# Performance work log

Hardware: AMD Instinct MI355X
Metric: run time of the kernel (lower is better)

The kernel has to match this reference:

```python
import jax, jax.numpy as jnp
import numpy as np

B, D, U = 4096, 1024, 1024  # batch, complex input dim, units


def _bias(u):
    # unit_forget_bias: zeros with forget-gate slice (i,f,c,o ordering) set to 1
    return jnp.zeros((4 * u,), jnp.float32).at[u:2 * u].set(1.0)


def setup_inputs() -> dict:
    key = jax.random.key(0)
    ks = jax.random.split(key, 7)
    s = 0.02  # kernel init scale
    return {
        "inputs": jax.random.normal(ks[0], (B, 2 * D), jnp.float32),
        "h_tm1": jax.random.normal(ks[1], (B, 2 * U), jnp.float32),
        "c_tm1": jax.random.normal(ks[2], (B, 2 * U), jnp.float32),
        "real_kernel": s * jax.random.normal(ks[3], (D, 4 * U), jnp.float32),
        "imaginary_kernel": s * jax.random.normal(ks[4], (D, 4 * U), jnp.float32),
        "real_recurrent_kernel": s * jax.random.normal(ks[5], (U, 4 * U), jnp.float32),
        "imaginary_recurrent_kernel": s * jax.random.normal(ks[6], (U, 4 * U), jnp.float32),
        "real_bias": _bias(U),
        "imaginary_bias": _bias(U),
    }


def hard_sigmoid(x):
    # keras hard_sigmoid: clip(0.2*x + 0.5, 0, 1)
    return jnp.clip(0.2 * x + 0.5, 0.0, 1.0)


def reference(inputs, h_tm1, c_tm1, real_kernel, imaginary_kernel,
              real_recurrent_kernel, imaginary_recurrent_kernel,
              real_bias, imaginary_bias):
    d = real_kernel.shape[0]
    u = real_recurrent_kernel.shape[0]
    xr, xi = inputs[:, :d], inputs[:, d:]          # [B,D] real/imag
    hr, hi = h_tm1[:, :u], h_tm1[:, u:]            # [B,U]
    # x @ [[R,-I],[I,R]] == [xr@R + xi@I, xi@R - xr@I]; done once over all 4 gates
    zr = xr @ real_kernel + xi @ imaginary_kernel \
         + hr @ real_recurrent_kernel + hi @ imaginary_recurrent_kernel + real_bias      # [B,4U]
    zi = xi @ real_kernel - xr @ imaginary_kernel \
         + hi @ real_recurrent_kernel - hr @ imaginary_recurrent_kernel + imaginary_bias  # [B,4U]

    def gate(g):  # concatenated real|imag pre-activation for gate g (i,f,c,o)
        s = slice(g * u, (g + 1) * u)
        return jnp.concatenate([zr[:, s], zi[:, s]], axis=-1)  # [B,2U]

    i = hard_sigmoid(gate(0))
    f = hard_sigmoid(gate(1))
    c = f * c_tm1 + i * jnp.tanh(gate(2))
    o = hard_sigmoid(gate(3))
    h = o * jnp.tanh(c)
    return h, c
```

## Files before the change

kernel.cpp:

```cpp
#include <hip/hip_runtime.h>

typedef unsigned short u16;
typedef unsigned int   u32;

typedef __bf16 bf16x8 __attribute__((ext_vector_type(8)));
typedef float  f32x4  __attribute__((ext_vector_type(4)));

typedef const __attribute__((address_space(1))) u32 GAS;
typedef __attribute__((address_space(3))) u32 LAS;

__device__ __forceinline__ u16 f2bf(float f) {
  u32 u = __builtin_bit_cast(u32, f);
  return (u16)((u + 0x7FFFu + ((u >> 16) & 1u)) >> 16);
}

__global__ __launch_bounds__(256) void build_x_k(
    const float* __restrict__ inp, const float* __restrict__ h,
    u16* __restrict__ X4) {
  __shared__ float t[64 * 65];
  const int tid = threadIdx.x;
  const int tx = tid & 15, ty = tid >> 4;
  const int m0 = blockIdx.y * 64, k0 = blockIdx.x * 64;
  const int sel = k0 >> 10;
  const int kc = k0 & 1023;
  const float* s1 = (sel < 2) ? inp : h;
  const int c1 = (sel & 1) * 1024 + kc;
#pragma unroll
  for (int rr = 0; rr < 4; ++rr) {
    const int m = rr * 16 + ty;
    float4 v = *(const float4*)&s1[(size_t)(m0 + m) * 2048 + c1 + tx * 4];
    t[(tx * 4 + 0) * 65 + m] = v.x;
    t[(tx * 4 + 1) * 65 + m] = v.y;
    t[(tx * 4 + 2) * 65 + m] = v.z;
    t[(tx * 4 + 3) * 65 + m] = v.w;
  }
  __syncthreads();
#pragma unroll
  for (int rep = 0; rep < 2; ++rep) {
    const int cell = rep * 256 + tid;
    const int kblk = cell >> 6, m = cell & 63;
    union { u16 s[8]; uint4 v; } tmp;
#pragma unroll
    for (int i = 0; i < 8; ++i) tmp.s[i] = f2bf(t[(kblk * 8 + i) * 65 + m]);
    *(uint4*)&X4[((size_t)(k0 / 8 + kblk) * 4096 + m0 + m) * 8] = tmp.v;
  }
}

__global__ __launch_bounds__(256) void build_w_k(
    const float* __restrict__ Kr, const float* __restrict__ Ki,
    const float* __restrict__ Rr, const float* __restrict__ Ri,
    u16* __restrict__ W4) {
  __shared__ float t[4 * 1032];
  const int tid = threadIdx.x;
  const int tx = tid & 15, ty = tid >> 4;
  const int yb = blockIdx.y;
  const int hh = yb >> 6, jhi = yb & 63;
  const int k0 = blockIdx.x * 64;
  const int kq = k0 >> 10;
  const int krow = k0 & 1023;
  const int jbase = jhi * 16;
  const float* sA;
  float sg = 1.0f;
  if (hh == 0) {
    sA = (kq == 0) ? Kr : (kq == 1) ? Ki : (kq == 2) ? Rr : Ri;
  } else {
    sA = (kq == 0) ? Ki : (kq == 1) ? Kr : (kq == 2) ? Ri : Rr;
    if ((kq & 1) == 0) sg = -1.0f;
  }
#pragma unroll
  for (int g = 0; g < 4; ++g) {
    const int cs = g * 1024 + jbase + tx;
#pragma unroll
    for (int rr = 0; rr < 4; ++rr) {
      const int k = rr * 16 + ty;
      t[g * 1032 + k * 16 + tx] = sg * sA[(size_t)(krow + k) * 4096 + cs];
    }
  }
  __syncthreads();
#pragma unroll
  for (int rep = 0; rep < 2; ++rep) {
    const int cell = rep * 256 + tid;
    const int kblk = cell >> 6, n = cell & 63;
    const int g = n >> 4, jlo = n & 15;
    union { u16 s[8]; uint4 v; } tmp;
#pragma unroll
    for (int i = 0; i < 8; ++i)
      tmp.s[i] = f2bf(t[g * 1032 + (kblk * 8 + i) * 16 + jlo]);
    *(uint4*)&W4[((size_t)(k0 / 8 + kblk) * 8192 + (size_t)hh * 4096 +
                  (size_t)jhi * 64 + n) * 8] = tmp.v;
  }
}

#define NKT 64

__global__ __launch_bounds__(512, 2) void clstm_gemm_k(
    const u16* __restrict__ X4, const u16* __restrict__ W4,
    const float* __restrict__ cprev, const float* __restrict__ rb,
    const float* __restrict__ ib, float* __restrict__ out) {
  __shared__ __align__(16) u16 lds[10][8192];
  const int tid = threadIdx.x;
  const int lane = tid & 63, wave = tid >> 6;
  const int wr = wave >> 2, wc = wave & 3;
  const int orig = blockIdx.x;
  const int wg = (orig & 7) * 64 + (orig >> 3);
  const int mb = wg >> 5, nb = wg & 31;
  const int m0 = mb * 256, n0 = nb * 256;
  const u16* L = &lds[0][0];

  f32x4 acc[8][4] = {};

  auto stageA = [&](int ktile, int hf, int slot) {
    const u16* s = X4 + ((size_t)(ktile * 8 + wave) * 4096 + m0 + hf * 128 + lane) * 8;
    __builtin_amdgcn_global_load_lds((GAS*)s, (LAS*)&lds[slot][(wave * 128) * 8], 16, 0, 0);
    __builtin_amdgcn_global_load_lds((GAS*)(s + 512), (LAS*)&lds[slot][(wave * 128 + 64) * 8], 16, 0, 0);
  };
  auto stageB = [&](int ktile, int hf, int slot) {
    const u16* s = W4 + ((size_t)(ktile * 8 + wave) * 8192 + n0 + hf * 128 + lane) * 8;
    __builtin_amdgcn_global_load_lds((GAS*)s, (LAS*)&lds[slot][(wave * 128) * 8], 16, 0, 0);
    __builtin_amdgcn_global_load_lds((GAS*)(s + 512), (LAS*)&lds[slot][(wave * 128 + 64) * 8], 16, 0, 0);
  };

  const int hi = lane >> 4, lo = lane & 15;
  const int abase = hi * 1024 + lo * 8;
  const int bbase = hi * 1024 + (wc & 1) * 512 + lo * 8;

  stageA(0, 0, 0); stageA(0, 1, 1);
  stageB(0, 0, 2); stageB(0, 1, 3);
  stageA(1, 0, 4); stageA(1, 1, 5);
  asm volatile("s_waitcnt vmcnt(4)" ::: "memory");
  __builtin_amdgcn_s_barrier();

  int rbs = 0, ss = 6;
  for (int kt = 0; kt < NKT; ++kt) {
    int sA = rbs + wr;             if (sA >= 10) sA -= 10;
    int sB = rbs + 2 + (wc >> 1);  if (sB >= 10) sB -= 10;
    const u16* LA = L + sA * 8192;
    const u16* LB = L + sB * 8192;
    bf16x8 av[4], bq[4];

#pragma unroll
    for (int mf = 0; mf < 4; ++mf)
      av[mf] = *(const bf16x8*)&LA[abase + mf * 128];
#pragma unroll
    for (int n = 0; n < 4; ++n)
      bq[n] = *(const bf16x8*)&LB[bbase + n * 128];
    if (kt + 1 < NKT) { stageB(kt + 1, 0, ss); ++ss; if (ss == 10) ss = 0; }
    __builtin_amdgcn_s_barrier();
    asm volatile("s_waitcnt lgkmcnt(0)" ::: "memory");
    __builtin_amdgcn_s_setprio(1);
#pragma unroll
    for (int mf = 0; mf < 4; ++mf)
#pragma unroll
      for (int n = 0; n < 4; ++n)
        acc[mf][n] = __builtin_amdgcn_mfma_f32_16x16x32_bf16(av[mf], bq[n], acc[mf][n], 0, 0, 0);
    __builtin_amdgcn_s_setprio(0);
    __builtin_amdgcn_s_barrier();

#pragma unroll
    for (int mf = 0; mf < 4; ++mf)
      av[mf] = *(const bf16x8*)&LA[abase + 512 + mf * 128];
    if (kt + 1 < NKT) { stageB(kt + 1, 1, ss); ++ss; if (ss == 10) ss = 0; }
    __builtin_amdgcn_s_barrier();
    asm volatile("s_waitcnt lgkmcnt(0)" ::: "memory");
    __builtin_amdgcn_s_setprio(1);
#pragma unroll
    for (int mf = 0; mf < 4; ++mf)
#pragma unroll
      for (int n = 0; n < 4; ++n)
        acc[4 + mf][n] = __builtin_amdgcn_mfma_f32_16x16x32_bf16(av[mf], bq[n], acc[4 + mf][n], 0, 0, 0);
    __builtin_amdgcn_s_setprio(0);
    __builtin_amdgcn_s_barrier();

#pragma unroll
    for (int mf = 0; mf < 4; ++mf)
      av[mf] = *(const bf16x8*)&LA[abase + 4096 + mf * 128];
#pragma unroll
    for (int n = 0; n < 4; ++n)
      bq[n] = *(const bf16x8*)&LB[bbase + 4096 + n * 128];
    if (kt + 2 < NKT) { stageA(kt + 2, 0, ss); ++ss; if (ss == 10) ss = 0; }
    __builtin_amdgcn_s_barrier();
    asm volatile("s_waitcnt lgkmcnt(0)" ::: "memory");
    __builtin_amdgcn_s_setprio(1);
#pragma unroll
    for (int mf = 0; mf < 4; ++mf)
#pragma unroll
      for (int n = 0; n < 4; ++n)
        acc[mf][n] = __builtin_amdgcn_mfma_f32_16x16x32_bf16(av[mf], bq[n], acc[mf][n], 0, 0, 0);
    __builtin_amdgcn_s_setprio(0);
    __builtin_amdgcn_s_barrier();

#pragma unroll
    for (int mf = 0; mf < 4; ++mf)
      av[mf] = *(const bf16x8*)&LA[abase + 4096 + 512 + mf * 128];
    if (kt + 2 < NKT) { stageA(kt + 2, 1, ss); ++ss; if (ss == 10) ss = 0; }
    if (kt < NKT - 2)       asm volatile("s_waitcnt vmcnt(4)" ::: "memory");
    else if (kt == NKT - 2) asm volatile("s_waitcnt vmcnt(0)" ::: "memory");
    __builtin_amdgcn_s_barrier();
    asm volatile("s_waitcnt lgkmcnt(0)" ::: "memory");
    __builtin_amdgcn_s_setprio(1);
#pragma unroll
    for (int mf = 0; mf < 4; ++mf)
#pragma unroll
      for (int n = 0; n < 4; ++n)
        acc[4 + mf][n] = __builtin_amdgcn_mfma_f32_16x16x32_bf16(av[mf], bq[n], acc[4 + mf][n], 0, 0, 0);
    __builtin_amdgcn_s_setprio(0);
    __builtin_amdgcn_s_barrier();

    rbs += 4; if (rbs >= 10) rbs -= 10;
  }

  const int half = nb >> 4;
  const int j = ((nb & 15) * 4 + wc) * 16 + lo;
  const float* bias = half ? ib : rb;
  float bs[4];
#pragma unroll
  for (int g = 0; g < 4; ++g) bs[g] = bias[g * 1024 + j];
#pragma unroll
  for (int mf8 = 0; mf8 < 8; ++mf8) {
    const int rowb = m0 + wr * 128 + mf8 * 16 + hi * 4;
#pragma unroll
    for (int r = 0; r < 4; ++r) {
      const size_t row = (size_t)(rowb + r);
      const float z0 = acc[mf8][0][r] + bs[0];
      const float z1 = acc[mf8][1][r] + bs[1];
      const float z2 = acc[mf8][2][r] + bs[2];
      const float z3 = acc[mf8][3][r] + bs[3];
      const float ig = fminf(fmaxf(0.2f * z0 + 0.5f, 0.0f), 1.0f);
      const float fg = fminf(fmaxf(0.2f * z1 + 0.5f, 0.0f), 1.0f);
      const float og = fminf(fmaxf(0.2f * z3 + 0.5f, 0.0f), 1.0f);
      const float cp = cprev[row * 2048 + half * 1024 + j];
      const float cn = fg * cp + ig * tanhf(z2);
      const float hn = og * tanhf(cn);
      out[row * 2048 + half * 1024 + j] = hn;
      out[(size_t)8388608 + row * 2048 + half * 1024 + j] = cn;
    }
  }
}

extern "C" void kernel_launch(void* const* d_in, const int* in_sizes, int n_in,
                              void* d_out, int out_size, void* d_ws, size_t ws_size,
                              hipStream_t stream) {
  const float* inputs = (const float*)d_in[0];
  const float* h_tm1  = (const float*)d_in[1];
  const float* c_tm1  = (const float*)d_in[2];
  const float* Kr     = (const float*)d_in[3];
  const float* Ki     = (const float*)d_in[4];
  const float* Rr     = (const float*)d_in[5];
  const float* Ri     = (const float*)d_in[6];
  const float* rb     = (const float*)d_in[7];
  const float* ib     = (const float*)d_in[8];
  float* out = (float*)d_out;

  u16* X4 = (u16*)d_ws;
  u16* W4 = X4 + (size_t)512 * 4096 * 8;

  build_x_k<<<dim3(64, 64), 256, 0, stream>>>(inputs, h_tm1, X4);
  build_w_k<<<dim3(64, 128), 256, 0, stream>>>(Kr, Ki, Rr, Ri, W4);
  clstm_gemm_k<<<dim3(512, 1), 512, 0, stream>>>(X4, W4, c_tm1, rb, ib, out);
}
```

Before: 311.6 us.

## Double-buffer LDS fragment registers to overlap ds_reads with MFMA phases

Restructures the main GEMM loop so register fragments are ping-ponged (avA/avB, bqA/bqB). LDS reads for the next phase, including the next k-tile's first fragments, are issued before the current MFMA block, with partial lgkmcnt waits instead of full drains. Barriers per phase drop from two to one and the vmcnt threshold is adjusted. This is meant to hide LDS latency behind matrix math, at the cost of more VGPRs and more delicate correctness around buffer reuse and wait counts.

```diff
diff --git a/kernel.cpp b/kernel.cpp
--- a/kernel.cpp
+++ b/kernel.cpp
@@ -93,6 +93,16 @@
 
 #define NKT 64
 
+#define MFMA16(AV, BQ, Q)                                                   \
+  __builtin_amdgcn_s_setprio(1);                                            \
+  _Pragma("unroll")                                                         \
+  for (int mf = 0; mf < 4; ++mf)                                            \
+    _Pragma("unroll")                                                       \
+    for (int n = 0; n < 4; ++n)                                             \
+      acc[(Q) * 4 + mf][n] = __builtin_amdgcn_mfma_f32_16x16x32_bf16(       \
+          AV[mf], BQ[n], acc[(Q) * 4 + mf][n], 0, 0, 0);                    \
+  __builtin_amdgcn_s_setprio(0);
+
 __global__ __launch_bounds__(512, 2) void clstm_gemm_k(
     const u16* __restrict__ X4, const u16* __restrict__ W4,
     const float* __restrict__ cprev, const float* __restrict__ rb,
@@ -130,81 +140,65 @@
   asm volatile("s_waitcnt vmcnt(4)" ::: "memory");
   __builtin_amdgcn_s_barrier();
 
+  bf16x8 avA[4], avB[4], bqA[4], bqB[4];
+  {
+    const u16* LA = L + (size_t)(0 + wr) * 8192;
+    const u16* LB = L + (size_t)(2 + (wc >> 1)) * 8192;
+#pragma unroll
+    for (int mf = 0; mf < 4; ++mf) avA[mf] = *(const bf16x8*)&LA[abase + mf * 128];
+#pragma unroll
+    for (int n = 0; n < 4; ++n)    bqA[n]  = *(const bf16x8*)&LB[bbase + n * 128];
+  }
+
   int rbs = 0, ss = 6;
   for (int kt = 0; kt < NKT; ++kt) {
     int sA = rbs + wr;             if (sA >= 10) sA -= 10;
     int sB = rbs + 2 + (wc >> 1);  if (sB >= 10) sB -= 10;
-    const u16* LA = L + sA * 8192;
-    const u16* LB = L + sB * 8192;
-    bf16x8 av[4], bq[4];
-
-#pragma unroll
-    for (int mf = 0; mf < 4; ++mf)
-      av[mf] = *(const bf16x8*)&LA[abase + mf * 128];
-#pragma unroll
-    for (int n = 0; n < 4; ++n)
-      bq[n] = *(const bf16x8*)&LB[bbase + n * 128];
+    const u16* LA = L + (size_t)sA * 8192;
+    const u16* LB = L + (size_t)sB * 8192;
+
+    __builtin_amdgcn_s_barrier();
     if (kt + 1 < NKT) { stageB(kt + 1, 0, ss); ++ss; if (ss == 10) ss = 0; }
-    __builtin_amdgcn_s_barrier();
-    asm volatile("s_waitcnt lgkmcnt(0)" ::: "memory");
-    __builtin_amdgcn_s_setprio(1);
-#pragma unroll
-    for (int mf = 0; mf < 4; ++mf)
-#pragma unroll
-      for (int n = 0; n < 4; ++n)
-        acc[mf][n] = __builtin_amdgcn_mfma_f32_16x16x32_bf16(av[mf], bq[n], acc[mf][n], 0, 0, 0);
-    __builtin_amdgcn_s_setprio(0);
-    __builtin_amdgcn_s_barrier();
-
-#pragma unroll
-    for (int mf = 0; mf < 4; ++mf)
-      av[mf] = *(const bf16x8*)&LA[abase + 512 + mf * 128];
+#pragma unroll
+    for (int mf = 0; mf < 4; ++mf) avB[mf] = *(const bf16x8*)&LA[abase + 512 + mf * 128];
+    asm volatile("s_waitcnt lgkmcnt(4)" ::: "memory");
+    MFMA16(avA, bqA, 0)
+
+    __builtin_amdgcn_s_barrier();
     if (kt + 1 < NKT) { stageB(kt + 1, 1, ss); ++ss; if (ss == 10) ss = 0; }
-    __builtin_amdgcn_s_barrier();
-    asm volatile("s_waitcnt lgkmcnt(0)" ::: "memory");
-    __builtin_amdgcn_s_setprio(1);
-#pragma unroll
-    for (int mf = 0; mf < 4; ++mf)
-#pragma unroll
-      for (int n = 0; n < 4; ++n)
-        acc[4 + mf][n] = __builtin_amdgcn_mfma_f32_16x16x32_bf16(av[mf], bq[n], acc[4 + mf][n], 0, 0, 0);
-    __builtin_amdgcn_s_setprio(0);
-    __builtin_amdgcn_s_barrier();
-
-#pragma unroll
-    for (int mf = 0; mf < 4; ++mf)
-      av[mf] = *(const bf16x8*)&LA[abase + 4096 + mf * 128];
-#pragma unroll
-    for (int n = 0; n < 4; ++n)
-      bq[n] = *(const bf16x8*)&LB[bbase + 4096 + n * 128];
+#pragma unroll
+    for (int mf = 0; mf < 4; ++mf) avA[mf] = *(const bf16x8*)&LA[abase + 4096 + mf * 128];
+#pragma unroll
+    for (int n = 0; n < 4; ++n)    bqB[n]  = *(const bf16x8*)&LB[bbase + 4096 + n * 128];
+    asm volatile("s_waitcnt lgkmcnt(8)" ::: "memory");
+    MFMA16(avB, bqA, 1)
+
+    __builtin_amdgcn_s_barrier();
     if (kt + 2 < NKT) { stageA(kt + 2, 0, ss); ++ss; if (ss == 10) ss = 0; }
-    __builtin_amdgcn_s_barrier();
-    asm volatile("s_waitcnt lgkmcnt(0)" ::: "memory");
-    __builtin_amdgcn_s_setprio(1);
-#pragma unroll
-    for (int mf = 0; mf < 4; ++mf)
-#pragma unroll
-      for (int n = 0; n < 4; ++n)
-        acc[mf][n] = __builtin_amdgcn_mfma_f32_16x16x32_bf16(av[mf], bq[n], acc[mf][n], 0, 0, 0);
-    __builtin_amdgcn_s_setprio(0);
-    __builtin_amdgcn_s_barrier();
-
-#pragma unroll
-    for (int mf = 0; mf < 4; ++mf)
-      av[mf] = *(const bf16x8*)&LA[abase + 4096 + 512 + mf * 128];
+#pragma unroll
+    for (int mf = 0; mf < 4; ++mf) avB[mf] = *(const bf16x8*)&LA[abase + 4096 + 512 + mf * 128];
+    asm volatile("s_waitcnt lgkmcnt(4)" ::: "memory");
+    MFMA16(avA, bqB, 0)
+
+    if (kt < NKT - 2)       asm volatile("s_waitcnt vmcnt(2)" ::: "memory");
+    else if (kt == NKT - 2) asm volatile("s_waitcnt vmcnt(0)" ::: "memory");
+    __builtin_amdgcn_s_barrier();
     if (kt + 2 < NKT) { stageA(kt + 2, 1, ss); ++ss; if (ss == 10) ss = 0; }
-    if (kt < NKT - 2)       asm volatile("s_waitcnt vmcnt(4)" ::: "memory");
-    else if (kt == NKT - 2) asm volatile("s_waitcnt vmcnt(0)" ::: "memory");
-    __builtin_amdgcn_s_barrier();
-    asm volatile("s_waitcnt lgkmcnt(0)" ::: "memory");
-    __builtin_amdgcn_s_setprio(1);
-#pragma unroll
-    for (int mf = 0; mf < 4; ++mf)
-#pragma unroll
-      for (int n = 0; n < 4; ++n)
-        acc[4 + mf][n] = __builtin_amdgcn_mfma_f32_16x16x32_bf16(av[mf], bq[n], acc[4 + mf][n], 0, 0, 0);
-    __builtin_amdgcn_s_setprio(0);
-    __builtin_amdgcn_s_barrier();
+    if (kt + 1 < NKT) {
+      int rbs2 = rbs + 4; if (rbs2 >= 10) rbs2 -= 10;
+      int sA2 = rbs2 + wr;             if (sA2 >= 10) sA2 -= 10;
+      int sB2 = rbs2 + 2 + (wc >> 1);  if (sB2 >= 10) sB2 -= 10;
+      const u16* LA2 = L + (size_t)sA2 * 8192;
+      const u16* LB2 = L + (size_t)sB2 * 8192;
+#pragma unroll
+      for (int mf = 0; mf < 4; ++mf) avA[mf] = *(const bf16x8*)&LA2[abase + mf * 128];
+#pragma unroll
+      for (int n = 0; n < 4; ++n)    bqA[n]  = *(const bf16x8*)&LB2[bbase + n * 128];
+      asm volatile("s_waitcnt lgkmcnt(8)" ::: "memory");
+    } else {
+      asm volatile("s_waitcnt lgkmcnt(0)" ::: "memory");
+    }
+    MFMA16(avB, bqB, 1)
 
     rbs += 4; if (rbs >= 10) rbs -= 10;
   }
```

Measured after the change: 307.0 us. No clear change (-1.5%).
